# Kernel tuning notes

Measured on AMD Instinct MI355X. Metric: run time of the kernel, lower is better.

Reference implementation:

```python
import jax, jax.numpy as jnp
import numpy as np

N_NODES = 100000
N_EDGES = 1600000
IN_DIM = 256
HID = 128
N_LAYERS = 4
OUT_DIM = 7
LAMDA = 0.5
LN_EPS = 1e-5


def setup_inputs() -> dict:
    key = jax.random.key(0)
    ks = jax.random.split(key, 12)
    x = jax.random.normal(ks[0], (N_NODES, IN_DIM), jnp.float32)
    edge_index = jax.random.randint(ks[1], (2, N_EDGES), 0, N_NODES, dtype=jnp.int32)

    def unif(k, shape, fan_out):
        s = 1.0 / np.sqrt(fan_out)
        return jax.random.uniform(k, shape, jnp.float32, -s, s)

    W_proj = unif(ks[2], (IN_DIM, HID), HID)
    b_proj = unif(ks[3], (HID,), HID)
    gamma = jnp.ones((HID,), jnp.float32)
    beta = jnp.zeros((HID,), jnp.float32)
    q_w = unif(ks[4], (HID, 1), 1)
    q_b = unif(ks[5], (1,), 1)
    conv_w = unif(ks[6], (N_LAYERS, HID, HID), HID)
    cls_w = unif(ks[7], (HID, OUT_DIM), OUT_DIM)
    cls_b = unif(ks[8], (OUT_DIM,), OUT_DIM)
    return {"x": x, "edge_index": edge_index, "W_proj": W_proj, "b_proj": b_proj,
            "gamma": gamma, "beta": beta, "q_w": q_w, "q_b": q_b,
            "conv_w": conv_w, "cls_w": cls_w, "cls_b": cls_b}


def reference(x, edge_index, W_proj, b_proj, gamma, beta, q_w, q_b, conv_w, cls_w, cls_b):
    n = x.shape[0]
    row, col = edge_index[0], edge_index[1]

    # symmetric normalization: D^-1/2 A D^-1/2 with unit edge data (duplicates sum)
    deg = jax.ops.segment_sum(jnp.ones(row.shape[0], x.dtype), row, num_segments=n)
    deg = jnp.where(deg == 0, jnp.ones_like(deg), deg)  # (row_sum==0)*1 + row_sum
    d_inv_sqrt = deg ** -0.5
    ew = d_inv_sqrt[row] * d_inv_sqrt[col]  # [E]

    def spmm(h):  # out[r] += ew * h[c]
        return jax.ops.segment_sum(ew[:, None] * h[col], row, num_segments=n)

    def layernorm(h):
        mu = jnp.mean(h, axis=-1, keepdims=True)
        var = jnp.mean((h - mu) ** 2, axis=-1, keepdims=True)
        return gamma * (h - mu) * jax.lax.rsqrt(var + LN_EPS) + beta

    h0 = layernorm(x @ W_proj + b_proj)  # project + layernorm
    h = h0
    for i in range(conv_w.shape[0]):
        # dropout is identity in eval mode
        s = jax.nn.sigmoid(h @ q_w + q_b - 1.0)  # [N,1] learned gate
        theta = LAMDA / (i + 1)
        hi = spmm(h)
        support = (1.0 - s) * hi + s * h0  # AOR blend (variant=False -> r == support)
        out = theta * (support @ conv_w[i]) + (1.0 - theta) * support  # DLR
        h = layernorm(jax.nn.relu(out))
    return h @ cls_w + cls_b
```

## Files before the change

kernel.cpp:

```cpp
#include <hip/hip_runtime.h>
#include <hip/hip_bf16.h>
#include <hip/hip_fp16.h>
#include <stdint.h>

#define N_NODES 100000
#define N_EDGES 1600000
#define IN_DIM 256
#define HID 128
#define N_LAYERS 4
#define OUT_DIM 7
#define LN_EPS 1e-5f

#define SCAN_B 1024
#define SCAN_NB ((N_NODES + SCAN_B - 1) / SCAN_B)

#define BSHIFT 6
#define BROWS 64
#define NBK 1563
#define BCAP 1408

typedef __attribute__((ext_vector_type(8))) short bf16x8;
typedef __attribute__((ext_vector_type(4))) float f32x4;

__device__ inline float bf2f1(uint16_t u) {
    union { uint32_t i; float f; } a; a.i = ((uint32_t)u) << 16; return a.f;
}
__device__ inline uint16_t f2bf(float f) {
    union { float f; uint32_t i; } a; a.f = f;
    uint32_t lsb = (a.i >> 16) & 1u;
    a.i += 0x7fffu + lsb;
    return (uint16_t)(a.i >> 16);
}
__device__ inline uint32_t packq(float a, float b, float qinv) {
    int qa = __float2int_rn(a * qinv);
    int qb = __float2int_rn(b * qinv);
    return ((uint32_t)(uint16_t)(short)qa) | (((uint32_t)(uint16_t)(short)qb) << 16);
}

__global__ void k_detect(const uint32_t* __restrict__ W, int* __restrict__ flag) {
    if (threadIdx.x == 0 && blockIdx.x == 0) {
        int cnt = 0;
        for (int i = 0; i < 64; i++) {
            uint32_t lo = W[i] & 0xffffu;
            uint32_t ex = (lo >> 7) & 0xff;
            if (ex >= 0x60 && ex < 0x7c) cnt++;
        }
        *flag = (cnt < 32) ? 1 : 0;
    }
}

__global__ __launch_bounds__(256) void k_cvt(const void* a0, const void* a1, const void* a2,
                                             const void* a3, const void* a4, const void* a5,
                                             const void* a6, const void* a7, const void* a8,
                                             float* __restrict__ dst, const int* __restrict__ flag) {
    int t = blockIdx.x * 256 + threadIdx.x;
    if (t >= 99720) return;
    const void* src; int i; int off;
    if      (t < 32768) { src = a0; i = t;         off = 0;     }
    else if (t < 32896) { src = a1; i = t - 32768; off = 32768; }
    else if (t < 33024) { src = a2; i = t - 32896; off = 32896; }
    else if (t < 33152) { src = a3; i = t - 33024; off = 33024; }
    else if (t < 33280) { src = a4; i = t - 33152; off = 33152; }
    else if (t < 33281) { src = a5; i = t - 33280; off = 33280; }
    else if (t < 98817) { src = a6; i = t - 33281; off = 33296; }
    else if (t < 99713) { src = a7; i = t - 98817; off = 98832; }
    else                { src = a8; i = t - 99713; off = 99728; }
    float v;
    if (*flag) v = ((const float*)src)[i];
    else       v = bf2f1(((const uint16_t*)src)[i]);
    dst[off + i] = v;
}

__global__ __launch_bounds__(256) void k_wsplit(const float* __restrict__ stg,
                                                uint16_t* __restrict__ wpThi, uint16_t* __restrict__ wpTlo,
                                                uint16_t* __restrict__ cwThi, uint16_t* __restrict__ cwTlo) {
    int t = blockIdx.x * 256 + threadIdx.x;
    if (t >= 32768 + 65536) return;
    float v; size_t dst; uint16_t *ha, *la;
    if (t < 32768) {
        int k = t >> 7, c = t & 127;
        v = stg[t];
        dst = (size_t)c * 256 + k; ha = wpThi; la = wpTlo;
    } else {
        int u = t - 32768;
        int L = u >> 14, rem = u & 16383;
        int k = rem >> 7, c = rem & 127;
        v = stg[33296 + u];
        dst = (size_t)L * 16384 + (size_t)c * 128 + k; ha = cwThi; la = cwTlo;
    }
    uint16_t hb = f2bf(v);
    uint16_t lb = f2bf(v - bf2f1(hb));
    ha[dst] = hb; la[dst] = lb;
}


__global__ __launch_bounds__(256) void k_part(const int* __restrict__ row, const int* __restrict__ col,
                                              int* __restrict__ bcnt, int2* __restrict__ eb) {
    int e = blockIdx.x * 256 + threadIdx.x;
    if (e >= N_EDGES) return;
    int r = row[e], c = col[e];
    int b = r >> BSHIFT;
    int pos = atomicAdd(&bcnt[b], 1);
    if (pos < BCAP) eb[(size_t)b * BCAP + pos] = make_int2(r, c);
}

__global__ __launch_bounds__(256) void k_bdeg(const int2* __restrict__ eb, const int* __restrict__ bcnt,
                                              int* __restrict__ deg) {
    __shared__ int ld[BROWS];
    int b = blockIdx.x, tid = threadIdx.x;
    if (tid < BROWS) ld[tid] = 0;
    __syncthreads();
    int n = bcnt[b]; if (n > BCAP) n = BCAP;
    const int2* base = eb + (size_t)b * BCAP;
    for (int i = tid; i < n; i += 256) atomicAdd(&ld[base[i].x & (BROWS - 1)], 1);
    __syncthreads();
    int r = (b << BSHIFT) + tid;
    if (tid < BROWS && r < N_NODES) deg[r] = ld[tid];
}

__global__ __launch_bounds__(SCAN_B) void k_scan1(const int* __restrict__ deg,
                                                  int* __restrict__ incl, int* __restrict__ bsum) {
    __shared__ int sm[SCAN_B];
    int t = threadIdx.x;
    int i = blockIdx.x * SCAN_B + t;
    int v = (i < N_NODES) ? deg[i] : 0;
    sm[t] = v;
    __syncthreads();
    for (int off = 1; off < SCAN_B; off <<= 1) {
        int add = (t >= off) ? sm[t - off] : 0;
        __syncthreads();
        sm[t] += add;
        __syncthreads();
    }
    if (i < N_NODES) incl[i] = sm[t];
    if (t == SCAN_B - 1) bsum[blockIdx.x] = sm[t];
}

__global__ __launch_bounds__(128) void k_scan2(const int* __restrict__ bsum, int* __restrict__ boff) {
    __shared__ int s[SCAN_NB];
    int t = threadIdx.x;
    if (t < SCAN_NB) s[t] = bsum[t];
    __syncthreads();
    if (t == 0) {
        int run = 0;
        for (int b = 0; b < SCAN_NB; b++) { int v = s[b]; s[b] = run; run += v; }
    }
    __syncthreads();
    if (t < SCAN_NB) boff[t] = s[t];
}

__global__ __launch_bounds__(256) void k_scan3(const int* __restrict__ deg, const int* __restrict__ incl,
                                               const int* __restrict__ boff,
                                               int* __restrict__ rp, float* __restrict__ dis) {
    int i = blockIdx.x * 256 + threadIdx.x;
    if (i >= N_NODES) return;
    int d = deg[i];
    int excl = boff[i / SCAN_B] + incl[i] - d;
    rp[i] = excl;
    if (i == N_NODES - 1) rp[N_NODES] = excl + d;
    dis[i] = rsqrtf((float)(d > 0 ? d : 1));
}

__global__ __launch_bounds__(256) void k_bscat(const int2* __restrict__ eb, const int* __restrict__ bcnt,
                                               const int* __restrict__ rp, int* __restrict__ edc) {
    __shared__ int lcur[BROWS];
    int b = blockIdx.x, tid = threadIdx.x;
    int row0 = b << BSHIFT;
    if (tid < BROWS) lcur[tid] = (row0 + tid < N_NODES) ? rp[row0 + tid] : 0;
    __syncthreads();
    int n = bcnt[b]; if (n > BCAP) n = BCAP;
    const int2* base = eb + (size_t)b * BCAP;
    for (int i = tid; i < n; i += 256) {
        int2 rc = base[i];
        int pos = atomicAdd(&lcur[rc.x & (BROWS - 1)], 1);
        edc[pos] = rc.y;
    }
}


__global__ __launch_bounds__(256) void k_spmm(const uint32_t* __restrict__ Hq,
                                              const float* __restrict__ ScD,
                                              const float* __restrict__ H0,
                                              const int* __restrict__ rp,
                                              const int* __restrict__ edc,
                                              const float* __restrict__ S,
                                              const float* __restrict__ dis,
                                              float* __restrict__ Sup) {
    int wid  = (blockIdx.x * 256 + threadIdx.x) >> 6;
    int lane = threadIdx.x & 63;
    if (wid >= N_NODES) return;

    float s  = S[wid];
    float dr = dis[wid];

    int p0 = rp[wid], p1 = rp[wid + 1];
    float ax = 0.f, ay = 0.f;
    int p = p0;
    for (; p + 4 <= p1; p += 4) {
        int c0 = edc[p], c1 = edc[p + 1], c2 = edc[p + 2], c3 = edc[p + 3];
        uint32_t u0 = Hq[(size_t)c0 * 64 + lane];
        uint32_t u1 = Hq[(size_t)c1 * 64 + lane];
        uint32_t u2 = Hq[(size_t)c2 * 64 + lane];
        uint32_t u3 = Hq[(size_t)c3 * 64 + lane];
        float w0 = ScD[c0], w1 = ScD[c1], w2 = ScD[c2], w3 = ScD[c3];
        ax += w0 * (float)((int)(u0 << 16) >> 16) + w1 * (float)((int)(u1 << 16) >> 16)
            + w2 * (float)((int)(u2 << 16) >> 16) + w3 * (float)((int)(u3 << 16) >> 16);
        ay += w0 * (float)((int)u0 >> 16) + w1 * (float)((int)u1 >> 16)
            + w2 * (float)((int)u2 >> 16) + w3 * (float)((int)u3 >> 16);
    }
    for (; p < p1; p++) {
        int c = edc[p];
        uint32_t u = Hq[(size_t)c * 64 + lane];
        float w = ScD[c];
        ax += w * (float)((int)(u << 16) >> 16);
        ay += w * (float)((int)u >> 16);
    }
    float h0x = H0[(size_t)wid * 128 + lane];
    float h0y = H0[(size_t)wid * 128 + 64 + lane];
    float f = (1.f - s) * dr;
    Sup[(size_t)wid * 128 + lane]      = f * ax + s * h0x;
    Sup[(size_t)wid * 128 + 64 + lane] = f * ay + s * h0y;
}


template <int KD, int MODE, int WH, int WQ>
__global__ __launch_bounds__(256) void k_gemm_mfma(
    const void* __restrict__ Araw,
    const uint16_t* __restrict__ WThi,
    const uint16_t* __restrict__ WTlo,
    const float* __restrict__ bias, const float* __restrict__ gamma,
    const float* __restrict__ beta, const float* __restrict__ qw,
    const float* __restrict__ qb, float theta, const int* __restrict__ flag,
    const float* __restrict__ dis,
    float* __restrict__ Hout, uint32_t* __restrict__ Hq,
    float* __restrict__ Sc, float* __restrict__ S)
{
    __shared__ __align__(16) uint16_t sAhi[64 * 64];
    __shared__ __align__(16) uint16_t sAlo[64 * 64];
    __shared__ __align__(16) uint16_t sBhi[128 * 64];
    __shared__ __align__(16) uint16_t sBlo[128 * 64];

    const int tid  = threadIdx.x;
    const int lane = tid & 63;
    const int wv   = tid >> 6;
    const int li   = lane & 15;
    const int lg   = lane >> 4;
    const size_t row0 = (size_t)blockIdx.x * 64;
    const int f32in = (MODE == 0) ? *flag : 1;

    f32x4 acc[8];
#pragma unroll
    for (int ct = 0; ct < 8; ct++) acc[ct] = (f32x4){0.f, 0.f, 0.f, 0.f};

    for (int kc = 0; kc < KD / 64; kc++) {
        __syncthreads();
#pragma unroll
        for (int it = 0; it < 2; it++) {
            int s  = tid + it * 256;
            int r  = s >> 3, sl = s & 7;
            size_t rg = row0 + r; if (rg >= N_NODES) rg = N_NODES - 1;
            uint4 vh, vl;
            if (f32in) {
                const float* p = (const float*)Araw + rg * KD + kc * 64 + sl * 8;
                float4 u0 = *(const float4*)p;
                float4 u1 = *(const float4*)(p + 4);
                float f[8] = {u0.x, u0.y, u0.z, u0.w, u1.x, u1.y, u1.z, u1.w};
                uint32_t hw[8], lw[8];
#pragma unroll
                for (int j = 0; j < 8; j++) {
                    uint16_t hb = f2bf(f[j]);
                    uint16_t lb = f2bf(f[j] - bf2f1(hb));
                    hw[j] = hb; lw[j] = lb;
                }
                vh.x = hw[0] | (hw[1] << 16); vh.y = hw[2] | (hw[3] << 16);
                vh.z = hw[4] | (hw[5] << 16); vh.w = hw[6] | (hw[7] << 16);
                vl.x = lw[0] | (lw[1] << 16); vl.y = lw[2] | (lw[3] << 16);
                vl.z = lw[4] | (lw[5] << 16); vl.w = lw[6] | (lw[7] << 16);
            } else {
                vh = *(const uint4*)((const uint16_t*)Araw + rg * KD + kc * 64 + sl * 8);
                vl.x = 0u; vl.y = 0u; vl.z = 0u; vl.w = 0u;
            }
            uint32_t byte = (uint32_t)(r * 128 + sl * 16) ^ (uint32_t)((r & 7) << 4);
            *(uint4*)((char*)sAhi + byte) = vh;
            *(uint4*)((char*)sAlo + byte) = vl;
        }
#pragma unroll
        for (int it = 0; it < 4; it++) {
            int s = tid + it * 256;
            int r = s >> 3, sl = s & 7;
            size_t gsrc = (size_t)r * KD + kc * 64 + sl * 8;
            uint4 vh = *(const uint4*)(WThi + gsrc);
            uint4 vl = *(const uint4*)(WTlo + gsrc);
            uint32_t byte = (uint32_t)(r * 128 + sl * 16) ^ (uint32_t)((r & 7) << 4);
            *(uint4*)((char*)sBhi + byte) = vh;
            *(uint4*)((char*)sBlo + byte) = vl;
        }
        __syncthreads();
#pragma unroll
        for (int ks = 0; ks < 2; ks++) {
            int arow = wv * 16 + li;
            uint32_t ab = (uint32_t)(arow * 128 + ks * 64 + lg * 16) ^ (uint32_t)((arow & 7) << 4);
            bf16x8 ah = *(const bf16x8*)((const char*)sAhi + ab);
            bf16x8 al = *(const bf16x8*)((const char*)sAlo + ab);
#pragma unroll
            for (int ct = 0; ct < 8; ct++) {
                int brow = ct * 16 + li;
                uint32_t bb = (uint32_t)(brow * 128 + ks * 64 + lg * 16) ^ (uint32_t)((brow & 7) << 4);
                bf16x8 bh = *(const bf16x8*)((const char*)sBhi + bb);
                bf16x8 bl = *(const bf16x8*)((const char*)sBlo + bb);
                acc[ct] = __builtin_amdgcn_mfma_f32_16x16x32_bf16(ah, bh, acc[ct], 0, 0, 0);
                acc[ct] = __builtin_amdgcn_mfma_f32_16x16x32_bf16(ah, bl, acc[ct], 0, 0, 0);
                acc[ct] = __builtin_amdgcn_mfma_f32_16x16x32_bf16(al, bh, acc[ct], 0, 0, 0);
            }
        }
    }

    float gm[8], bt[8], qv[8], bi[8];
#pragma unroll
    for (int ct = 0; ct < 8; ct++) {
        int c = ct * 16 + li;
        gm[ct] = gamma[c]; bt[ct] = beta[c]; qv[ct] = qw[c];
        bi[ct] = (MODE == 0) ? bias[c] : 0.f;
    }
    const float qbv = qb[0];
    const float om  = 1.f - theta;
    const float* Af = (const float*)Araw;

#pragma unroll
    for (int r = 0; r < 4; r++) {
        int rowl  = wv * 16 + lg * 4 + r;
        size_t rg = row0 + rowl;
        size_t rc = (rg < N_NODES) ? rg : (N_NODES - 1);
        float v[8];
        if (MODE == 0) {
#pragma unroll
            for (int ct = 0; ct < 8; ct++) v[ct] = acc[ct][r] + bi[ct];
        } else {
#pragma unroll
            for (int ct = 0; ct < 8; ct++) {
                float sv = Af[rc * KD + ct * 16 + li];
                float o  = theta * acc[ct][r] + om * sv;
                v[ct] = o > 0.f ? o : 0.f;
            }
        }
        float sum = 0.f, sq = 0.f;
#pragma unroll
        for (int ct = 0; ct < 8; ct++) { sum += v[ct]; sq += v[ct] * v[ct]; }
        sum += __shfl_xor(sum, 1); sum += __shfl_xor(sum, 2);
        sum += __shfl_xor(sum, 4); sum += __shfl_xor(sum, 8);
        sq  += __shfl_xor(sq, 1);  sq  += __shfl_xor(sq, 2);
        sq  += __shfl_xor(sq, 4);  sq  += __shfl_xor(sq, 8);
        float mu  = sum * (1.f / 128.f);
        float var = fmaxf(sq * (1.f / 128.f) - mu * mu, 0.f);
        float rs  = rsqrtf(var + LN_EPS);
        float y[8];
#pragma unroll
        for (int ct = 0; ct < 8; ct++) y[ct] = gm[ct] * (v[ct] - mu) * rs + bt[ct];

        if (WQ) {
            float zd = 0.f, am = 0.f;
#pragma unroll
            for (int ct = 0; ct < 8; ct++) { zd += y[ct] * qv[ct]; am = fmaxf(am, fabsf(y[ct])); }
            zd += __shfl_xor(zd, 1); zd += __shfl_xor(zd, 2);
            zd += __shfl_xor(zd, 4); zd += __shfl_xor(zd, 8);
            am = fmaxf(am, __shfl_xor(am, 1)); am = fmaxf(am, __shfl_xor(am, 2));
            am = fmaxf(am, __shfl_xor(am, 4)); am = fmaxf(am, __shfl_xor(am, 8));
            float amc  = fmaxf(am, 1e-20f);
            float qinv = 32767.f / amc;
            if (rg < N_NODES) {
                uint32_t* mq = Hq + rg * 64;
#pragma unroll
                for (int ct = 0; ct < 4; ct++)
                    mq[ct * 16 + li] = packq(y[ct], y[ct + 4], qinv);
                if (li == 0) {
                    Sc[rg] = amc * (1.f / 32767.f) * dis[rg];
                    S[rg]  = 1.f / (1.f + __expf(-(zd + qbv - 1.f)));
                }
            }
        }
        if (WH && rg < N_NODES) {
            float* dst = Hout + rg * 128;
#pragma unroll
            for (int ct = 0; ct < 8; ct++) dst[ct * 16 + li] = y[ct];
        }
    }
}


__global__ __launch_bounds__(256) void k_cls(const float* __restrict__ H,
                                             const float* __restrict__ Wc,
                                             const float* __restrict__ bc,
                                             const int* __restrict__ flag,
                                             void* __restrict__ out) {
    __shared__ float wS[128][8];
    int tid = threadIdx.x;
    for (int idx = tid; idx < 128 * 7; idx += 256) wS[idx / 7][idx % 7] = Wc[idx];
    __syncthreads();
    int isf32 = *flag;
    int gid = blockIdx.x * 256 + tid;
    int n = gid >> 3, j = gid & 7;
    if (n >= N_NODES || j >= OUT_DIM) return;
    const float4* hr = (const float4*)(H + (size_t)n * 128);
    float acc = bc[j];
#pragma unroll
    for (int k4 = 0; k4 < 32; k4++) {
        float4 h4 = hr[k4];
        acc += h4.x * wS[4 * k4][j]     + h4.y * wS[4 * k4 + 1][j]
             + h4.z * wS[4 * k4 + 2][j] + h4.w * wS[4 * k4 + 3][j];
    }
    size_t oi = (size_t)n * OUT_DIM + j;
    if (isf32) ((float*)out)[oi] = acc;
    else       ((uint16_t*)out)[oi] = f2bf(acc);
}


extern "C" void kernel_launch(void* const* d_in, const int* in_sizes, int n_in,
                              void* d_out, int out_size, void* d_ws, size_t ws_size,
                              hipStream_t stream) {
    const void* x_raw = d_in[0];
    const int*  ei    = (const int*)d_in[1];
    const int* row = ei;
    const int* col = ei + N_EDGES;

    char* ws = (char*)d_ws;
    size_t off = 0;
    auto alloc = [&](size_t b) { void* p = ws + off; off = (off + b + 255) & ~(size_t)255; return p; };
    int*      flag = (int*)alloc(4);
    float*    stgf = (float*)alloc((size_t)99744 * 4);
    int*      deg  = (int*)alloc((size_t)N_NODES * 4);
    int*      rp   = (int*)alloc(((size_t)N_NODES + 1) * 4);
    float*    dis  = (float*)alloc((size_t)N_NODES * 4);
    int*      incl = (int*)alloc((size_t)N_NODES * 4);
    int*      bsum = (int*)alloc((size_t)SCAN_NB * 4);
    int*      boff = (int*)alloc((size_t)SCAN_NB * 4);
    int*      bcnt = (int*)alloc((size_t)NBK * 4);
    int*      edc  = (int*)alloc((size_t)N_EDGES * 4);
    float*    h0   = (float*)alloc((size_t)N_NODES * HID * 4);
    float*    sup  = (float*)alloc((size_t)N_NODES * HID * 4);
    uint32_t* hq   = (uint32_t*)alloc((size_t)N_NODES * 64 * 4);
    float*    Scq  = (float*)alloc((size_t)N_NODES * 4);
    float*    Sg   = (float*)alloc((size_t)N_NODES * 4);
    uint16_t* wpThi = (uint16_t*)alloc((size_t)32768 * 2);
    uint16_t* wpTlo = (uint16_t*)alloc((size_t)32768 * 2);
    uint16_t* cwThi = (uint16_t*)alloc((size_t)65536 * 2);
    uint16_t* cwTlo = (uint16_t*)alloc((size_t)65536 * 2);
    int2*     eb   = (int2*)h0;

    const float* bp  = stgf + 32768;
    const float* gm  = stgf + 32896;
    const float* bt  = stgf + 33024;
    const float* qw  = stgf + 33152;
    const float* qb  = stgf + 33280;
    const float* clw = stgf + 98832;
    const float* clb = stgf + 99728;

    k_detect<<<1, 64, 0, stream>>>((const uint32_t*)d_in[2], flag);
    k_cvt<<<(99720 + 255) / 256, 256, 0, stream>>>(d_in[2], d_in[3], d_in[4], d_in[5], d_in[6],
                                                   d_in[7], d_in[8], d_in[9], d_in[10], stgf, flag);
    k_wsplit<<<(98304 + 255) / 256, 256, 0, stream>>>(stgf, wpThi, wpTlo, cwThi, cwTlo);

    hipMemsetAsync(bcnt, 0, (size_t)NBK * 4, stream);
    k_part<<<(N_EDGES + 255) / 256, 256, 0, stream>>>(row, col, bcnt, eb);
    k_bdeg<<<NBK, 256, 0, stream>>>(eb, bcnt, deg);
    k_scan1<<<SCAN_NB, SCAN_B, 0, stream>>>(deg, incl, bsum);
    k_scan2<<<1, 128, 0, stream>>>(bsum, boff);
    k_scan3<<<(N_NODES + 255) / 256, 256, 0, stream>>>(deg, incl, boff, rp, dis);
    k_bscat<<<NBK, 256, 0, stream>>>(eb, bcnt, rp, edc);

    const int gemm_grid = (N_NODES + 63) / 64;
    k_gemm_mfma<IN_DIM, 0, 1, 1><<<gemm_grid, 256, 0, stream>>>(
        x_raw, wpThi, wpTlo, bp, gm, bt, qw, qb, 0.f, flag, dis, h0, hq, Scq, Sg);

    for (int i = 0; i < N_LAYERS; i++) {
        k_spmm<<<(N_NODES + 3) / 4, 256, 0, stream>>>(hq, Scq, h0, rp, edc, Sg, dis, sup);
        float theta = 0.5f / (float)(i + 1);
        const uint16_t* whi = cwThi + (size_t)i * 16384;
        const uint16_t* wlo = cwTlo + (size_t)i * 16384;
        if (i < N_LAYERS - 1) {
            k_gemm_mfma<HID, 1, 0, 1><<<gemm_grid, 256, 0, stream>>>(
                sup, whi, wlo, nullptr, gm, bt, qw, qb, theta, flag, dis, sup, hq, Scq, Sg);
        } else {
            k_gemm_mfma<HID, 1, 1, 0><<<gemm_grid, 256, 0, stream>>>(
                sup, whi, wlo, nullptr, gm, bt, qw, qb, theta, flag, dis, sup, hq, Scq, Sg);
        }
    }
    k_cls<<<((size_t)N_NODES * 8 + 255) / 256, 256, 0, stream>>>(sup, clw, clb, flag, d_out);
}
```

Measured before the change: 928.3 us.

## Replace capped bucket partition with chunked histogram counting sort for CSR build

Swaps the global-atomic bucket partition with a fixed per-bucket capacity, and the separate degree and scan kernels, for a two-pass counting sort. Per-chunk shared-memory histograms over 64-row buckets are scanned across chunks and buckets, then edges are scattered with packed 32-bit row/col keys. A final per-bucket kernel computes degrees, row pointers, normalization and CSR column order locally. This removes contended global atomics, the capacity overflow risk and several scan launches, but reads the edge list twice and uses only 98 blocks for the histogram and scatter passes.

New measurement: 755.0 us. 18.7% less time.

```diff
diff --git a/kernel.cpp b/kernel.cpp
--- a/kernel.cpp
+++ b/kernel.cpp
@@ -11,13 +11,11 @@
 #define OUT_DIM 7
 #define LN_EPS 1e-5f
 
-#define SCAN_B 1024
-#define SCAN_NB ((N_NODES + SCAN_B - 1) / SCAN_B)
-
 #define BSHIFT 6
 #define BROWS 64
 #define NBK 1563
-#define BCAP 1408
+#define CHUNK 16384
+#define NCH ((N_EDGES + CHUNK - 1) / CHUNK)
 
 typedef __attribute__((ext_vector_type(8))) short bf16x8;
 typedef __attribute__((ext_vector_type(4))) float f32x4;
@@ -94,86 +92,115 @@
 }
 
 
-__global__ __launch_bounds__(256) void k_part(const int* __restrict__ row, const int* __restrict__ col,
-                                              int* __restrict__ bcnt, int2* __restrict__ eb) {
-    int e = blockIdx.x * 256 + threadIdx.x;
-    if (e >= N_EDGES) return;
-    int r = row[e], c = col[e];
-    int b = r >> BSHIFT;
-    int pos = atomicAdd(&bcnt[b], 1);
-    if (pos < BCAP) eb[(size_t)b * BCAP + pos] = make_int2(r, c);
-}
-
-__global__ __launch_bounds__(256) void k_bdeg(const int2* __restrict__ eb, const int* __restrict__ bcnt,
-                                              int* __restrict__ deg) {
-    __shared__ int ld[BROWS];
+__global__ __launch_bounds__(256) void k_hist(const int* __restrict__ row, int* __restrict__ hist) {
+    __shared__ int lh[NBK];
     int b = blockIdx.x, tid = threadIdx.x;
-    if (tid < BROWS) ld[tid] = 0;
-    __syncthreads();
-    int n = bcnt[b]; if (n > BCAP) n = BCAP;
-    const int2* base = eb + (size_t)b * BCAP;
-    for (int i = tid; i < n; i += 256) atomicAdd(&ld[base[i].x & (BROWS - 1)], 1);
-    __syncthreads();
-    int r = (b << BSHIFT) + tid;
-    if (tid < BROWS && r < N_NODES) deg[r] = ld[tid];
-}
-
-__global__ __launch_bounds__(SCAN_B) void k_scan1(const int* __restrict__ deg,
-                                                  int* __restrict__ incl, int* __restrict__ bsum) {
-    __shared__ int sm[SCAN_B];
+    for (int i = tid; i < NBK; i += 256) lh[i] = 0;
+    __syncthreads();
+    int e0 = b * CHUNK;
+    int lim = N_EDGES - e0; if (lim > CHUNK) lim = CHUNK;
+    for (int i = tid; i < lim; i += 256) atomicAdd(&lh[row[e0 + i] >> BSHIFT], 1);
+    __syncthreads();
+    for (int i = tid; i < NBK; i += 256) hist[(size_t)b * NBK + i] = lh[i];
+}
+
+__global__ __launch_bounds__(128) void k_hscan(int* __restrict__ hist, int* __restrict__ totB) {
+    __shared__ int s[128];
+    int bkt = blockIdx.x, t = threadIdx.x;
+    int v = (t < NCH) ? hist[(size_t)t * NBK + bkt] : 0;
+    s[t] = v;
+    __syncthreads();
+    for (int off = 1; off < 128; off <<= 1) {
+        int add = (t >= off) ? s[t - off] : 0;
+        __syncthreads();
+        s[t] += add;
+        __syncthreads();
+    }
+    if (t < NCH) hist[(size_t)t * NBK + bkt] = s[t] - v;
+    if (t == 127) totB[bkt] = s[127];
+}
+
+__global__ __launch_bounds__(256) void k_bscan(const int* __restrict__ totB,
+                                               int* __restrict__ boffB, int* __restrict__ rp) {
+    __shared__ int ps[256];
     int t = threadIdx.x;
-    int i = blockIdx.x * SCAN_B + t;
-    int v = (i < N_NODES) ? deg[i] : 0;
-    sm[t] = v;
-    __syncthreads();
-    for (int off = 1; off < SCAN_B; off <<= 1) {
-        int add = (t >= off) ? sm[t - off] : 0;
+    const int STRIP = 7;
+    int base = t * STRIP;
+    int loc[STRIP]; int sum = 0;
+#pragma unroll
+    for (int j = 0; j < STRIP; j++) {
+        int idx = base + j;
+        int v = (idx < NBK) ? totB[idx] : 0;
+        loc[j] = sum; sum += v;
+    }
+    ps[t] = sum;
+    __syncthreads();
+    int v = ps[t];
+    for (int off = 1; off < 256; off <<= 1) {
+        int add = (t >= off) ? ps[t - off] : 0;
         __syncthreads();
-        sm[t] += add;
+        ps[t] += add;
         __syncthreads();
     }
-    if (i < N_NODES) incl[i] = sm[t];
-    if (t == SCAN_B - 1) bsum[blockIdx.x] = sm[t];
-}
-
-__global__ __launch_bounds__(128) void k_scan2(const int* __restrict__ bsum, int* __restrict__ boff) {
-    __shared__ int s[SCAN_NB];
-    int t = threadIdx.x;
-    if (t < SCAN_NB) s[t] = bsum[t];
-    __syncthreads();
-    if (t == 0) {
-        int run = 0;
-        for (int b = 0; b < SCAN_NB; b++) { int v = s[b]; s[b] = run; run += v; }
-    }
-    __syncthreads();
-    if (t < SCAN_NB) boff[t] = s[t];
-}
-
-__global__ __launch_bounds__(256) void k_scan3(const int* __restrict__ deg, const int* __restrict__ incl,
-                                               const int* __restrict__ boff,
-                                               int* __restrict__ rp, float* __restrict__ dis) {
-    int i = blockIdx.x * 256 + threadIdx.x;
-    if (i >= N_NODES) return;
-    int d = deg[i];
-    int excl = boff[i / SCAN_B] + incl[i] - d;
-    rp[i] = excl;
-    if (i == N_NODES - 1) rp[N_NODES] = excl + d;
-    dis[i] = rsqrtf((float)(d > 0 ? d : 1));
-}
-
-__global__ __launch_bounds__(256) void k_bscat(const int2* __restrict__ eb, const int* __restrict__ bcnt,
-                                               const int* __restrict__ rp, int* __restrict__ edc) {
+    int excl = ps[t] - v;
+#pragma unroll
+    for (int j = 0; j < STRIP; j++) {
+        int idx = base + j;
+        if (idx < NBK) boffB[idx] = excl + loc[j];
+    }
+    if (t == 0) { boffB[NBK] = N_EDGES; rp[N_NODES] = N_EDGES; }
+}
+
+__global__ __launch_bounds__(256) void k_sortscat(const int* __restrict__ row, const int* __restrict__ col,
+                                                  const int* __restrict__ hist, const int* __restrict__ boffB,
+                                                  uint32_t* __restrict__ ebp) {
+    __shared__ int dbase[NBK];
+    __shared__ int lcnt[NBK];
+    int b = blockIdx.x, tid = threadIdx.x;
+    for (int i = tid; i < NBK; i += 256) {
+        dbase[i] = boffB[i] + hist[(size_t)b * NBK + i];
+        lcnt[i] = 0;
+    }
+    __syncthreads();
+    int e0 = b * CHUNK;
+    int lim = N_EDGES - e0; if (lim > CHUNK) lim = CHUNK;
+    for (int i = tid; i < lim; i += 256) {
+        int r = row[e0 + i], c = col[e0 + i];
+        int bk = r >> BSHIFT;
+        int rank = atomicAdd(&lcnt[bk], 1);
+        ebp[dbase[bk] + rank] = ((uint32_t)(r & (BROWS - 1)) << 17) | (uint32_t)c;
+    }
+}
+
+__global__ __launch_bounds__(256) void k_bfin(const uint32_t* __restrict__ ebp, const int* __restrict__ boffB,
+                                              int* __restrict__ rp, float* __restrict__ dis,
+                                              int* __restrict__ edc) {
+    __shared__ int ldeg[BROWS];
     __shared__ int lcur[BROWS];
     int b = blockIdx.x, tid = threadIdx.x;
+    int base = boffB[b];
+    int n = boffB[b + 1] - base;
+    if (tid < BROWS) ldeg[tid] = 0;
+    __syncthreads();
+    for (int i = tid; i < n; i += 256) atomicAdd(&ldeg[ebp[base + i] >> 17], 1);
+    __syncthreads();
+    if (tid == 0) {
+        int run = 0;
+        for (int r = 0; r < BROWS; r++) { int d = ldeg[r]; lcur[r] = run; run += d; }
+    }
+    __syncthreads();
     int row0 = b << BSHIFT;
-    if (tid < BROWS) lcur[tid] = (row0 + tid < N_NODES) ? rp[row0 + tid] : 0;
-    __syncthreads();
-    int n = bcnt[b]; if (n > BCAP) n = BCAP;
-    const int2* base = eb + (size_t)b * BCAP;
+    if (tid < BROWS && row0 + tid < N_NODES) {
+        int d = ldeg[tid];
+        rp[row0 + tid]  = base + lcur[tid];
+        dis[row0 + tid] = rsqrtf((float)(d > 0 ? d : 1));
+    }
+    __syncthreads();
     for (int i = tid; i < n; i += 256) {
-        int2 rc = base[i];
-        int pos = atomicAdd(&lcur[rc.x & (BROWS - 1)], 1);
-        edc[pos] = rc.y;
+        uint32_t pk = ebp[base + i];
+        int r = pk >> 17;
+        int pos = atomicAdd(&lcur[r], 1);
+        edc[base + pos] = (int)(pk & 0x1FFFFu);
     }
 }
 
@@ -427,13 +454,11 @@
     auto alloc = [&](size_t b) { void* p = ws + off; off = (off + b + 255) & ~(size_t)255; return p; };
     int*      flag = (int*)alloc(4);
     float*    stgf = (float*)alloc((size_t)99744 * 4);
-    int*      deg  = (int*)alloc((size_t)N_NODES * 4);
     int*      rp   = (int*)alloc(((size_t)N_NODES + 1) * 4);
     float*    dis  = (float*)alloc((size_t)N_NODES * 4);
-    int*      incl = (int*)alloc((size_t)N_NODES * 4);
-    int*      bsum = (int*)alloc((size_t)SCAN_NB * 4);
-    int*      boff = (int*)alloc((size_t)SCAN_NB * 4);
-    int*      bcnt = (int*)alloc((size_t)NBK * 4);
+    int*      hist = (int*)alloc((size_t)NCH * NBK * 4);
+    int*      totB = (int*)alloc((size_t)NBK * 4);
+    int*      boffB= (int*)alloc(((size_t)NBK + 1) * 4);
     int*      edc  = (int*)alloc((size_t)N_EDGES * 4);
     float*    h0   = (float*)alloc((size_t)N_NODES * HID * 4);
     float*    sup  = (float*)alloc((size_t)N_NODES * HID * 4);
@@ -444,7 +469,7 @@
     uint16_t* wpTlo = (uint16_t*)alloc((size_t)32768 * 2);
     uint16_t* cwThi = (uint16_t*)alloc((size_t)65536 * 2);
     uint16_t* cwTlo = (uint16_t*)alloc((size_t)65536 * 2);
-    int2*     eb   = (int2*)h0;
+    uint32_t* ebp  = (uint32_t*)h0;
 
     const float* bp  = stgf + 32768;
     const float* gm  = stgf + 32896;
@@ -459,13 +484,11 @@
                                                    d_in[7], d_in[8], d_in[9], d_in[10], stgf, flag);
     k_wsplit<<<(98304 + 255) / 256, 256, 0, stream>>>(stgf, wpThi, wpTlo, cwThi, cwTlo);
 
-    hipMemsetAsync(bcnt, 0, (size_t)NBK * 4, stream);
-    k_part<<<(N_EDGES + 255) / 256, 256, 0, stream>>>(row, col, bcnt, eb);
-    k_bdeg<<<NBK, 256, 0, stream>>>(eb, bcnt, deg);
-    k_scan1<<<SCAN_NB, SCAN_B, 0, stream>>>(deg, incl, bsum);
-    k_scan2<<<1, 128, 0, stream>>>(bsum, boff);
-    k_scan3<<<(N_NODES + 255) / 256, 256, 0, stream>>>(deg, incl, boff, rp, dis);
-    k_bscat<<<NBK, 256, 0, stream>>>(eb, bcnt, rp, edc);
+    k_hist<<<NCH, 256, 0, stream>>>(row, hist);
+    k_hscan<<<NBK, 128, 0, stream>>>(hist, totB);
+    k_bscan<<<1, 256, 0, stream>>>(totB, boffB, rp);
+    k_sortscat<<<NCH, 256, 0, stream>>>(row, col, hist, boffB, ebp);
+    k_bfin<<<NBK, 256, 0, stream>>>(ebp, boffB, rp, dis, edc);
 
     const int gemm_grid = (N_NODES + 63) / 64;
     k_gemm_mfma<IN_DIM, 0, 1, 1><<<gemm_grid, 256, 0, stream>>>(
```
